# Performance work log

Hardware: AMD Instinct MI355X
Metric: run time of the kernel (lower is better)

The kernel has to match this reference:

```python
import jax, jax.numpy as jnp
import numpy as np

N_EXPERTS = 8
D_MODEL = 1024
D_FF = 2048
N_TOKENS = 4096
TOP_K = 2


def _init_expert_weight(key, shape):
    # matches torch init: bound = sqrt(3) * (sqrt(1/3)/sqrt(fan_in)) = 1/sqrt(fan_in)
    fan_in = shape[1]
    bound = 1.0 / np.sqrt(fan_in)
    return jax.random.uniform(key, shape, dtype=jnp.float32, minval=-bound, maxval=bound)


def setup_inputs() -> dict:
    key = jax.random.key(0)
    k_x, k_idx, k_w, k1, k2, k3 = jax.random.split(key, 6)
    x = jax.random.normal(k_x, (N_TOKENS, D_MODEL), dtype=jnp.float32)
    expert_indices = jax.random.randint(k_idx, (N_TOKENS, TOP_K), 0, N_EXPERTS)
    expert_weights = jax.random.uniform(k_w, (N_TOKENS, TOP_K), dtype=jnp.float32)
    w1 = _init_expert_weight(k1, (N_EXPERTS, D_MODEL, D_FF))
    w2 = _init_expert_weight(k2, (N_EXPERTS, D_MODEL, D_FF))
    w3 = _init_expert_weight(k3, (N_EXPERTS, D_FF, D_MODEL))
    return {"x": x, "expert_indices": expert_indices, "expert_weights": expert_weights,
            "w1": w1, "w2": w2, "w3": w3}


def reference(x, expert_indices, expert_weights, w1, w2, w3):
    # SwiGLU per expert, computed densely over all (token, expert) pairs,
    # then the top-k selected expert outputs are gathered and combined.
    # Mathematically identical to the padded-bmm dispatch/combine in the source.
    gate = jax.nn.silu(jnp.einsum('td,edf->tef', x, w1))   # [T, E, F]
    value = jnp.einsum('td,edf->tef', x, w2)               # [T, E, F]
    hidden = gate * value                                  # [T, E, F]
    out_e = jnp.einsum('tef,efd->ted', hidden, w3)         # [T, E, D]
    # gather each token's top-k expert outputs: [T, K, D]
    sel = jnp.take_along_axis(out_e, expert_indices[:, :, None], axis=1)
    return jnp.sum(sel * expert_weights[:, :, None], axis=1)  # [T, D]
```

## Files before the change

### kernel.cpp

```cpp
#include <hip/hip_runtime.h>
#include <hip/hip_bf16.h>

#define N_TOK   4096
#define DM      1024
#define DF      2048
#define NEXP    8
#define NPAIR   (N_TOK * 2)
#define BM      128
#define BN      128
#define BK      32
#define LDK     40

typedef __attribute__((ext_vector_type(8))) short bf16x8;
typedef __attribute__((ext_vector_type(4))) float f32x4;

__device__ __forceinline__ unsigned short to_bf16(float f) {
    unsigned u = __builtin_bit_cast(unsigned, f);
    unsigned r = (u + 0x7FFFu + ((u >> 16) & 1u)) >> 16;
    return (unsigned short)r;
}
__device__ __forceinline__ unsigned pk_bf16(float a, float b) {
    return (unsigned)to_bf16(a) | ((unsigned)to_bf16(b) << 16);
}
__device__ __forceinline__ void gld16(const unsigned short* g, unsigned short* l) {
    __builtin_amdgcn_global_load_lds(
        (const __attribute__((address_space(1))) unsigned int*)(g),
        (__attribute__((address_space(3))) unsigned int*)(l), 16, 0, 0);
}

__global__ void k_count(const int* __restrict__ eidx, int* __restrict__ meta) {
    int i = blockIdx.x * 256 + threadIdx.x;
    if (i < NPAIR) atomicAdd(&meta[eidx[i] & 7], 1);
}
__global__ void k_scan(int* __restrict__ meta) {
    if (threadIdx.x == 0) {
        int off = 0, mt = 0;
        for (int e = 0; e < NEXP; ++e) {
            meta[16 + e] = off; meta[25 + e] = mt;
            int c = meta[e];
            off += c; mt += (c + BM - 1) / BM;
        }
        meta[16 + NEXP] = off; meta[25 + NEXP] = mt; meta[34] = mt;
    }
}
__global__ void k_scatter(const int* __restrict__ eidx, int* __restrict__ meta,
                          int* __restrict__ rows) {
    int i = blockIdx.x * 256 + threadIdx.x;
    if (i < NPAIR) {
        int e = eidx[i] & 7;
        int p = meta[16 + e] + atomicAdd(&meta[8 + e], 1);
        rows[p] = i;
    }
}

__global__ __launch_bounds__(256)
void k_cvt_x(const float* __restrict__ x, unsigned short* __restrict__ xb) {
    int i = (blockIdx.x * 256 + threadIdx.x) * 8;
    float4 v0 = *(const float4*)(x + i);
    float4 v1 = *(const float4*)(x + i + 4);
    uint4 w;
    w.x = pk_bf16(v0.x, v0.y); w.y = pk_bf16(v0.z, v0.w);
    w.z = pk_bf16(v1.x, v1.y); w.w = pk_bf16(v1.z, v1.w);
    *(uint4*)(xb + i) = w;
}

__global__ __launch_bounds__(256)
void k_transpose(const float* __restrict__ src, unsigned short* __restrict__ dst,
                 int K, int F) {
    __shared__ __align__(16) unsigned short tile[64 * 80];
    const int e  = blockIdx.z;
    const int k0 = blockIdx.y * 64;
    const int f0 = blockIdx.x * 64;
    const int t  = threadIdx.x;
    const float* s = src + (size_t)e * K * F;
    unsigned short* d = dst + (size_t)e * K * F;
    const int fi = t & 63;
    const int kg = t >> 6;
    #pragma unroll
    for (int i = 0; i < 16; ++i) {
        int k = kg * 16 + i;
        tile[k * 80 + fi] = to_bf16(s[(size_t)(k0 + k) * F + f0 + fi]);
    }
    __syncthreads();
    const int kc = (t & 7) * 8;
    const int fo = t >> 3;
    #pragma unroll
    for (int j = 0; j < 2; ++j) {
        int f = fo + j * 32;
        unsigned short v[8];
        #pragma unroll
        for (int i = 0; i < 8; ++i) v[i] = tile[(kc + i) * 80 + f];
        uint4 w;
        w.x = (unsigned)v[0] | ((unsigned)v[1] << 16);
        w.y = (unsigned)v[2] | ((unsigned)v[3] << 16);
        w.z = (unsigned)v[4] | ((unsigned)v[5] << 16);
        w.w = (unsigned)v[6] | ((unsigned)v[7] << 16);
        *(uint4*)&d[(size_t)(f0 + f) * K + k0 + kc] = w;
    }
}

__global__ __launch_bounds__(256, 2)
void k_gemm1_bf(const unsigned short* __restrict__ xb,
                const unsigned short* __restrict__ w1t,
                const unsigned short* __restrict__ w2t,
                const int* __restrict__ meta,
                const int* __restrict__ rows,
                unsigned short* __restrict__ H)
{
    __shared__ __align__(16) unsigned short As [BM * BK];
    __shared__ __align__(16) unsigned short B1s[BN * BK];
    __shared__ __align__(16) unsigned short B2s[BN * BK];
    __shared__ int s_tok[BM];

    const int mt = blockIdx.y;
    if (mt >= meta[34]) return;
    int e = 0;
    #pragma unroll
    for (int i = 0; i < NEXP - 1; ++i) if (mt >= meta[25 + i + 1]) e = i + 1;
    const int rowEnd = meta[16 + e + 1];
    const int row0   = meta[16 + e] + (mt - meta[25 + e]) * BM;
    const int f0     = blockIdx.x * BN;
    const int tid    = threadIdx.x;

    if (tid < BM) {
        int gr = row0 + tid;
        s_tok[tid] = (gr < rowEnd) ? (rows[gr] >> 1) : 0;
    }
    __syncthreads();

    const int lane = tid & 63;
    const int wave = tid >> 6;
    const int r0 = wave * 32 + (lane >> 2);
    const int r1 = r0 + 16;
    const int kb = (lane & 3) * 8;
    const unsigned short* a_src0 = xb + (size_t)s_tok[r0] * DM + kb;
    const unsigned short* a_src1 = xb + (size_t)s_tok[r1] * DM + kb;
    const size_t wb = (size_t)e * DM * DF;
    const unsigned short* b1_src0 = w1t + wb + (size_t)(f0 + r0) * DM + kb;
    const unsigned short* b1_src1 = w1t + wb + (size_t)(f0 + r1) * DM + kb;
    const unsigned short* b2_src0 = w2t + wb + (size_t)(f0 + r0) * DM + kb;
    const unsigned short* b2_src1 = w2t + wb + (size_t)(f0 + r1) * DM + kb;
    unsigned short* As0  = &As [wave * 1024];
    unsigned short* As1  = &As [wave * 1024 + 512];
    unsigned short* B1s0 = &B1s[wave * 1024];
    unsigned short* B1s1 = &B1s[wave * 1024 + 512];
    unsigned short* B2s0 = &B2s[wave * 1024];
    unsigned short* B2s1 = &B2s[wave * 1024 + 512];

    f32x4 accg[4][4], accv[4][4];
    #pragma unroll
    for (int i = 0; i < 4; ++i)
        #pragma unroll
        for (int j = 0; j < 4; ++j) { accg[i][j] = (f32x4)0.f; accv[i][j] = (f32x4)0.f; }

    const int wm = (wave >> 1) * 64;
    const int wn = (wave & 1) * 64;
    const int am = lane & 15;
    const int ak = (lane >> 4) * 8;

    for (int k0 = 0; k0 < DM; k0 += BK) {
        gld16(a_src0 + k0, As0);
        gld16(a_src1 + k0, As1);
        gld16(b1_src0 + k0, B1s0);
        gld16(b1_src1 + k0, B1s1);
        gld16(b2_src0 + k0, B2s0);
        gld16(b2_src1 + k0, B2s1);
        __syncthreads();

        bf16x8 a[4], b1[4], b2[4];
        #pragma unroll
        for (int mi = 0; mi < 4; ++mi) a[mi] = *(const bf16x8*)&As[(wm + mi * 16 + am) * BK + ak];
        #pragma unroll
        for (int ni = 0; ni < 4; ++ni) {
            b1[ni] = *(const bf16x8*)&B1s[(wn + ni * 16 + am) * BK + ak];
            b2[ni] = *(const bf16x8*)&B2s[(wn + ni * 16 + am) * BK + ak];
        }
        #pragma unroll
        for (int mi = 0; mi < 4; ++mi)
            #pragma unroll
            for (int ni = 0; ni < 4; ++ni) {
                accg[mi][ni] = __builtin_amdgcn_mfma_f32_16x16x32_bf16(a[mi], b1[ni], accg[mi][ni], 0, 0, 0);
                accv[mi][ni] = __builtin_amdgcn_mfma_f32_16x16x32_bf16(a[mi], b2[ni], accv[mi][ni], 0, 0, 0);
            }
        __syncthreads();
    }

    const int cn = lane & 15;
    const int cq = (lane >> 4) * 4;
    #pragma unroll
    for (int mi = 0; mi < 4; ++mi) {
        #pragma unroll
        for (int r = 0; r < 4; ++r) {
            const int row = wm + mi * 16 + cq + r;
            const int gr  = row0 + row;
            if (gr < rowEnd) {
                unsigned short* dst = H + (size_t)gr * DF + f0 + wn;
                #pragma unroll
                for (int ni = 0; ni < 4; ++ni) {
                    float g = accg[mi][ni][r];
                    float v = accv[mi][ni][r];
                    float h = (g * v) / (1.f + __expf(-g));
                    dst[ni * 16 + cn] = to_bf16(h);
                }
            }
        }
    }
}

__global__ __launch_bounds__(256, 2)
void k_gemm2_bf(const unsigned short* __restrict__ H,
                const unsigned short* __restrict__ w3t,
                const int* __restrict__ meta,
                const int* __restrict__ rows,
                const float* __restrict__ ew,
                float* __restrict__ out)
{
    __shared__ __align__(16) unsigned short As[BM * BK];
    __shared__ __align__(16) unsigned short Bs[BN * BK];
    __shared__ int   s_tok[BM];
    __shared__ float s_w[BM];

    const int mt = blockIdx.y;
    if (mt >= meta[34]) return;
    int e = 0;
    #pragma unroll
    for (int i = 0; i < NEXP - 1; ++i) if (mt >= meta[25 + i + 1]) e = i + 1;
    const int rowEnd = meta[16 + e + 1];
    const int row0   = meta[16 + e] + (mt - meta[25 + e]) * BM;
    const int d0     = blockIdx.x * BN;
    const int tid    = threadIdx.x;

    if (tid < BM) {
        int gr = row0 + tid;
        if (gr < rowEnd) { int pr = rows[gr]; s_tok[tid] = pr >> 1; s_w[tid] = ew[pr]; }
        else             { s_tok[tid] = 0;    s_w[tid] = 0.f; }
    }
    __syncthreads();

    const int lane = tid & 63;
    const int wave = tid >> 6;
    const int r0 = wave * 32 + (lane >> 2);
    const int r1 = r0 + 16;
    const int kb = (lane & 3) * 8;
    int gr0 = row0 + r0; if (gr0 > NPAIR - 1) gr0 = NPAIR - 1;
    int gr1 = row0 + r1; if (gr1 > NPAIR - 1) gr1 = NPAIR - 1;
    const unsigned short* a_src0 = H + (size_t)gr0 * DF + kb;
    const unsigned short* a_src1 = H + (size_t)gr1 * DF + kb;
    const size_t wb = (size_t)e * DM * DF;
    const unsigned short* b_src0 = w3t + wb + (size_t)(d0 + r0) * DF + kb;
    const unsigned short* b_src1 = w3t + wb + (size_t)(d0 + r1) * DF + kb;
    unsigned short* As0 = &As[wave * 1024];
    unsigned short* As1 = &As[wave * 1024 + 512];
    unsigned short* Bs0 = &Bs[wave * 1024];
    unsigned short* Bs1 = &Bs[wave * 1024 + 512];

    f32x4 acc[4][4];
    #pragma unroll
    for (int i = 0; i < 4; ++i)
        #pragma unroll
        for (int j = 0; j < 4; ++j) acc[i][j] = (f32x4)0.f;

    const int wm = (wave >> 1) * 64;
    const int wn = (wave & 1) * 64;
    const int am = lane & 15;
    const int ak = (lane >> 4) * 8;

    for (int k0 = 0; k0 < DF; k0 += BK) {
        gld16(a_src0 + k0, As0);
        gld16(a_src1 + k0, As1);
        gld16(b_src0 + k0, Bs0);
        gld16(b_src1 + k0, Bs1);
        __syncthreads();

        bf16x8 a[4], b[4];
        #pragma unroll
        for (int mi = 0; mi < 4; ++mi) a[mi] = *(const bf16x8*)&As[(wm + mi * 16 + am) * BK + ak];
        #pragma unroll
        for (int ni = 0; ni < 4; ++ni) b[ni] = *(const bf16x8*)&Bs[(wn + ni * 16 + am) * BK + ak];
        #pragma unroll
        for (int mi = 0; mi < 4; ++mi)
            #pragma unroll
            for (int ni = 0; ni < 4; ++ni)
                acc[mi][ni] = __builtin_amdgcn_mfma_f32_16x16x32_bf16(a[mi], b[ni], acc[mi][ni], 0, 0, 0);
        __syncthreads();
    }

    const int cn = lane & 15;
    const int cq = (lane >> 4) * 4;
    #pragma unroll
    for (int mi = 0; mi < 4; ++mi) {
        #pragma unroll
        for (int r = 0; r < 4; ++r) {
            const int row = wm + mi * 16 + cq + r;
            const int gr  = row0 + row;
            if (gr < rowEnd) {
                const int   tok = s_tok[row];
                const float wgt = s_w[row];
                float* dst = out + (size_t)tok * DM + d0 + wn;
                #pragma unroll
                for (int ni = 0; ni < 4; ++ni)
                    atomicAdd(&dst[ni * 16 + cn], wgt * acc[mi][ni][r]);
            }
        }
    }
}

__global__ __launch_bounds__(256, 2)
void k_gemm1(const float* __restrict__ x, const float* __restrict__ w1,
             const float* __restrict__ w2, const int* __restrict__ meta,
             const int* __restrict__ rows, unsigned short* __restrict__ H)
{
    __shared__ unsigned short As[BM][LDK];
    __shared__ unsigned short B1s[BN][LDK];
    __shared__ unsigned short B2s[BN][LDK];
    __shared__ int s_tok[BM];
    const int mt = blockIdx.y;
    if (mt >= meta[34]) return;
    int e = 0;
    #pragma unroll
    for (int i = 0; i < NEXP - 1; ++i) if (mt >= meta[25 + i + 1]) e = i + 1;
    const int rowEnd = meta[16 + e + 1];
    const int row0   = meta[16 + e] + (mt - meta[25 + e]) * BM;
    const int f0     = blockIdx.x * BN;
    const int tid    = threadIdx.x;
    if (tid < BM) {
        int gr = row0 + tid;
        s_tok[tid] = (gr < rowEnd) ? (rows[gr] >> 1) : -1;
    }
    __syncthreads();
    const int ar = tid >> 1;
    const int ah = (tid & 1) * 16;
    const int a_tok = s_tok[ar];
    const float* a_src = x + (size_t)(a_tok < 0 ? 0 : a_tok) * DM + ah;
    const int bn_ = tid & 127;
    const int bk_ = (tid >> 7) * 16;
    const float* b1_src = w1 + (size_t)e * DM * DF + (size_t)bk_ * DF + f0 + bn_;
    const float* b2_src = w2 + (size_t)e * DM * DF + (size_t)bk_ * DF + f0 + bn_;
    f32x4 accg[4][4], accv[4][4];
    #pragma unroll
    for (int i = 0; i < 4; ++i)
        #pragma unroll
        for (int j = 0; j < 4; ++j) { accg[i][j] = (f32x4)0.f; accv[i][j] = (f32x4)0.f; }
    const int lane = tid & 63;
    const int wave = tid >> 6;
    const int wm = (wave >> 1) * 64;
    const int wn = (wave & 1) * 64;
    const int am = lane & 15;
    const int ak = (lane >> 4) * 8;
    for (int k0 = 0; k0 < DM; k0 += BK) {
        {
            const float* p = a_src + k0;
            #pragma unroll
            for (int jj = 0; jj < 4; ++jj) {
                float4 v;
                if (a_tok < 0) { v.x = v.y = v.z = v.w = 0.f; }
                else           { v = *(const float4*)(p + jj * 4); }
                uint2 w;
                w.x = pk_bf16(v.x, v.y); w.y = pk_bf16(v.z, v.w);
                *(uint2*)&As[ar][ah + jj * 4] = w;
            }
        }
        {
            const float* p1 = b1_src + (size_t)k0 * DF;
            const float* p2 = b2_src + (size_t)k0 * DF;
            #pragma unroll
            for (int c = 0; c < 2; ++c) {
                float v[8];
                #pragma unroll
                for (int j = 0; j < 8; ++j) v[j] = p1[(size_t)(c * 8 + j) * DF];
                uint4 w;
                w.x = pk_bf16(v[0], v[1]); w.y = pk_bf16(v[2], v[3]);
                w.z = pk_bf16(v[4], v[5]); w.w = pk_bf16(v[6], v[7]);
                *(uint4*)&B1s[bn_][bk_ + c * 8] = w;
            }
            #pragma unroll
            for (int c = 0; c < 2; ++c) {
                float v[8];
                #pragma unroll
                for (int j = 0; j < 8; ++j) v[j] = p2[(size_t)(c * 8 + j) * DF];
                uint4 w;
                w.x = pk_bf16(v[0], v[1]); w.y = pk_bf16(v[2], v[3]);
                w.z = pk_bf16(v[4], v[5]); w.w = pk_bf16(v[6], v[7]);
                *(uint4*)&B2s[bn_][bk_ + c * 8] = w;
            }
        }
        __syncthreads();
        bf16x8 a[4], b1[4], b2[4];
        #pragma unroll
        for (int mi = 0; mi < 4; ++mi) a[mi] = *(const bf16x8*)&As[wm + mi * 16 + am][ak];
        #pragma unroll
        for (int ni = 0; ni < 4; ++ni) {
            b1[ni] = *(const bf16x8*)&B1s[wn + ni * 16 + am][ak];
            b2[ni] = *(const bf16x8*)&B2s[wn + ni * 16 + am][ak];
        }
        #pragma unroll
        for (int mi = 0; mi < 4; ++mi)
            #pragma unroll
            for (int ni = 0; ni < 4; ++ni) {
                accg[mi][ni] = __builtin_amdgcn_mfma_f32_16x16x32_bf16(a[mi], b1[ni], accg[mi][ni], 0, 0, 0);
                accv[mi][ni] = __builtin_amdgcn_mfma_f32_16x16x32_bf16(a[mi], b2[ni], accv[mi][ni], 0, 0, 0);
            }
        __syncthreads();
    }
    const int cn = lane & 15;
    const int cq = (lane >> 4) * 4;
    #pragma unroll
    for (int mi = 0; mi < 4; ++mi) {
        #pragma unroll
        for (int r = 0; r < 4; ++r) {
            const int row = wm + mi * 16 + cq + r;
            const int gr  = row0 + row;
            if (gr < rowEnd) {
                unsigned short* dst = H + (size_t)gr * DF + f0 + wn;
                #pragma unroll
                for (int ni = 0; ni < 4; ++ni) {
                    float g = accg[mi][ni][r];
                    float v = accv[mi][ni][r];
                    float h = (g * v) / (1.f + __expf(-g));
                    dst[ni * 16 + cn] = to_bf16(h);
                }
            }
        }
    }
}

__global__ __launch_bounds__(256, 2)
void k_gemm2(const unsigned short* __restrict__ H, const float* __restrict__ w3,
             const int* __restrict__ meta, const int* __restrict__ rows,
             const float* __restrict__ ew, float* __restrict__ out)
{
    __shared__ unsigned short As[BM][LDK];
    __shared__ unsigned short Bs[BN][LDK];
    __shared__ int   s_tok[BM];
    __shared__ float s_w[BM];
    const int mt = blockIdx.y;
    if (mt >= meta[34]) return;
    int e = 0;
    #pragma unroll
    for (int i = 0; i < NEXP - 1; ++i) if (mt >= meta[25 + i + 1]) e = i + 1;
    const int rowEnd = meta[16 + e + 1];
    const int row0   = meta[16 + e] + (mt - meta[25 + e]) * BM;
    const int d0     = blockIdx.x * BN;
    const int tid    = threadIdx.x;
    if (tid < BM) {
        int gr = row0 + tid;
        if (gr < rowEnd) { int pr = rows[gr]; s_tok[tid] = pr >> 1; s_w[tid] = ew[pr]; }
        else             { s_tok[tid] = 0;    s_w[tid] = 0.f; }
    }
    __syncthreads();
    const int ar = tid >> 1;
    const int ah = (tid & 1) * 16;
    int a_row = row0 + ar; if (a_row >= NPAIR) a_row = NPAIR - 1;
    const unsigned short* a_src = H + (size_t)a_row * DF + ah;
    const int bn_ = tid & 127;
    const int bk_ = (tid >> 7) * 16;
    const float* b_src = w3 + (size_t)e * DF * DM + (size_t)bk_ * DM + d0 + bn_;
    f32x4 acc[4][4];
    #pragma unroll
    for (int i = 0; i < 4; ++i)
        #pragma unroll
        for (int j = 0; j < 4; ++j) acc[i][j] = (f32x4)0.f;
    const int lane = tid & 63;
    const int wave = tid >> 6;
    const int wm = (wave >> 1) * 64;
    const int wn = (wave & 1) * 64;
    const int am = lane & 15;
    const int ak = (lane >> 4) * 8;
    for (int k0 = 0; k0 < DF; k0 += BK) {
        *(uint4*)&As[ar][ah]     = *(const uint4*)(a_src + k0);
        *(uint4*)&As[ar][ah + 8] = *(const uint4*)(a_src + k0 + 8);
        {
            const float* p = b_src + (size_t)k0 * DM;
            #pragma unroll
            for (int c = 0; c < 2; ++c) {
                float v[8];
                #pragma unroll
                for (int j = 0; j < 8; ++j) v[j] = p[(size_t)(c * 8 + j) * DM];
                uint4 w;
                w.x = pk_bf16(v[0], v[1]); w.y = pk_bf16(v[2], v[3]);
                w.z = pk_bf16(v[4], v[5]); w.w = pk_bf16(v[6], v[7]);
                *(uint4*)&Bs[bn_][bk_ + c * 8] = w;
            }
        }
        __syncthreads();
        bf16x8 a[4], b[4];
        #pragma unroll
        for (int mi = 0; mi < 4; ++mi) a[mi] = *(const bf16x8*)&As[wm + mi * 16 + am][ak];
        #pragma unroll
        for (int ni = 0; ni < 4; ++ni) b[ni] = *(const bf16x8*)&Bs[wn + ni * 16 + am][ak];
        #pragma unroll
        for (int mi = 0; mi < 4; ++mi)
            #pragma unroll
            for (int ni = 0; ni < 4; ++ni)
                acc[mi][ni] = __builtin_amdgcn_mfma_f32_16x16x32_bf16(a[mi], b[ni], acc[mi][ni], 0, 0, 0);
        __syncthreads();
    }
    const int cn = lane & 15;
    const int cq = (lane >> 4) * 4;
    #pragma unroll
    for (int mi = 0; mi < 4; ++mi) {
        #pragma unroll
        for (int r = 0; r < 4; ++r) {
            const int row = wm + mi * 16 + cq + r;
            const int gr  = row0 + row;
            if (gr < rowEnd) {
                const int   tok = s_tok[row];
                const float wgt = s_w[row];
                float* dst = out + (size_t)tok * DM + d0 + wn;
                #pragma unroll
                for (int ni = 0; ni < 4; ++ni)
                    atomicAdd(&dst[ni * 16 + cn], wgt * acc[mi][ni][r]);
            }
        }
    }
}

__global__ __launch_bounds__(256)
void k_fallback(const float* __restrict__ x, const int* __restrict__ eidx,
                const float* __restrict__ ew, const float* __restrict__ w1,
                const float* __restrict__ w2, const float* __restrict__ w3,
                float* __restrict__ out)
{
    __shared__ float xs[DM];
    __shared__ float hs[DF];
    const int pair = blockIdx.x;
    const int t = pair >> 1;
    const int e = eidx[pair] & 7;
    const float wgt = ew[pair];
    const int tid = threadIdx.x;
    for (int i = tid; i < DM; i += 256) xs[i] = x[(size_t)t * DM + i];
    __syncthreads();
    for (int f = tid; f < DF; f += 256) {
        const float* c1 = w1 + (size_t)e * DM * DF + f;
        const float* c2 = w2 + (size_t)e * DM * DF + f;
        float g = 0.f, v = 0.f;
        for (int d = 0; d < DM; ++d) {
            float xv = xs[d];
            g += xv * c1[(size_t)d * DF];
            v += xv * c2[(size_t)d * DF];
        }
        hs[f] = (g * v) / (1.f + __expf(-g));
    }
    __syncthreads();
    for (int d = tid; d < DM; d += 256) {
        const float* c3 = w3 + (size_t)e * DF * DM + d;
        float o = 0.f;
        for (int f = 0; f < DF; ++f) o += hs[f] * c3[(size_t)f * DM];
        atomicAdd(&out[(size_t)t * DM + d], wgt * o);
    }
}

extern "C" void kernel_launch(void* const* d_in, const int* in_sizes, int n_in,
                              void* d_out, int out_size, void* d_ws, size_t ws_size,
                              hipStream_t stream)
{
    const float* x  = (const float*)d_in[0];
    const int*   ei = (const int*)  d_in[1];
    const float* ew = (const float*)d_in[2];
    const float* w1 = (const float*)d_in[3];
    const float* w2 = (const float*)d_in[4];
    const float* w3 = (const float*)d_in[5];
    float* out = (float*)d_out;

    (void)hipMemsetAsync(d_out, 0, (size_t)out_size * sizeof(float), stream);

    const size_t SZ_H  = (size_t)NPAIR * DF * 2;
    const size_t SZ_XB = (size_t)N_TOK * DM * 2;
    const size_t SZ_W  = (size_t)NEXP * DM * DF * 2;
    const size_t OFF_H  = 65536;
    const size_t OFF_XB = OFF_H + SZ_H;
    const size_t OFF_W1 = OFF_XB + SZ_XB;
    const size_t OFF_W2 = OFF_W1 + SZ_W;
    const size_t OFF_W3 = OFF_W2 + SZ_W;
    const size_t NEED_BIG   = OFF_W3 + SZ_W;
    const size_t NEED_SMALL = OFF_H + SZ_H;

    if (ws_size < NEED_SMALL) {
        k_fallback<<<NPAIR, 256, 0, stream>>>(x, ei, ew, w1, w2, w3, out);
        return;
    }

    int* meta = (int*)d_ws;
    int* rows = meta + 64;
    unsigned short* H = (unsigned short*)((char*)d_ws + OFF_H);

    (void)hipMemsetAsync(d_ws, 0, 64, stream);
    k_count  <<<NPAIR / 256, 256, 0, stream>>>(ei, meta);
    k_scan   <<<1, 64, 0, stream>>>(meta);
    k_scatter<<<NPAIR / 256, 256, 0, stream>>>(ei, meta, rows);

    if (ws_size >= NEED_BIG) {
        unsigned short* xb  = (unsigned short*)((char*)d_ws + OFF_XB);
        unsigned short* w1t = (unsigned short*)((char*)d_ws + OFF_W1);
        unsigned short* w2t = (unsigned short*)((char*)d_ws + OFF_W2);
        unsigned short* w3t = (unsigned short*)((char*)d_ws + OFF_W3);
        k_cvt_x<<<(N_TOK * DM) / 2048, 256, 0, stream>>>(x, xb);
        k_transpose<<<dim3(DF / 64, DM / 64, NEXP), 256, 0, stream>>>(w1, w1t, DM, DF);
        k_transpose<<<dim3(DF / 64, DM / 64, NEXP), 256, 0, stream>>>(w2, w2t, DM, DF);
        k_transpose<<<dim3(DM / 64, DF / 64, NEXP), 256, 0, stream>>>(w3, w3t, DF, DM);
        k_gemm1_bf<<<dim3(DF / BN, NPAIR / BM + NEXP), 256, 0, stream>>>(xb, w1t, w2t, meta, rows, H);
        k_gemm2_bf<<<dim3(DM / BN, NPAIR / BM + NEXP), 256, 0, stream>>>(H, w3t, meta, rows, ew, out);
    } else {
        k_gemm1<<<dim3(DF / BN, NPAIR / BM + NEXP), 256, 0, stream>>>(x, w1, w2, meta, rows, H);
        k_gemm2<<<dim3(DM / BN, NPAIR / BM + NEXP), 256, 0, stream>>>(H, w3, meta, rows, ew, out);
    }
}
```

Baseline: 490.3 us.

## Replace atomic combine with per-pair output buffer, fuse count/scan, vectorize transpose

```diff
diff --git a/kernel.cpp b/kernel.cpp
--- a/kernel.cpp
+++ b/kernel.cpp
@@ -28,28 +28,37 @@
         (__attribute__((address_space(3))) unsigned int*)(l), 16, 0, 0);
 }
 
-__global__ void k_count(const int* __restrict__ eidx, int* __restrict__ meta) {
-    int i = blockIdx.x * 256 + threadIdx.x;
-    if (i < NPAIR) atomicAdd(&meta[eidx[i] & 7], 1);
-}
-__global__ void k_scan(int* __restrict__ meta) {
-    if (threadIdx.x == 0) {
+__global__ __launch_bounds__(256)
+void k_countscan(const int* __restrict__ eidx, int* __restrict__ meta) {
+    __shared__ int hist[NEXP];
+    const int t = threadIdx.x;
+    if (t < NEXP) hist[t] = 0;
+    __syncthreads();
+    unsigned long long h = 0;
+    for (int i = t; i < NPAIR; i += 256) h += 1ull << ((eidx[i] & 7) * 8);
+    #pragma unroll
+    for (int e = 0; e < NEXP; ++e) {
+        int c = (int)((h >> (e * 8)) & 0xFF);
+        if (c) atomicAdd(&hist[e], c);
+    }
+    __syncthreads();
+    if (t == 0) {
         int off = 0, mt = 0;
         for (int e = 0; e < NEXP; ++e) {
-            meta[16 + e] = off; meta[25 + e] = mt;
-            int c = meta[e];
-            off += c; mt += (c + BM - 1) / BM;
+            meta[16 + e] = off; meta[25 + e] = mt; meta[8 + e] = 0;
+            off += hist[e]; mt += (hist[e] + BM - 1) / BM;
         }
         meta[16 + NEXP] = off; meta[25 + NEXP] = mt; meta[34] = mt;
     }
 }
 __global__ void k_scatter(const int* __restrict__ eidx, int* __restrict__ meta,
-                          int* __restrict__ rows) {
+                          int* __restrict__ rows, int* __restrict__ inv) {
     int i = blockIdx.x * 256 + threadIdx.x;
     if (i < NPAIR) {
         int e = eidx[i] & 7;
         int p = meta[16 + e] + atomicAdd(&meta[8 + e], 1);
         rows[p] = i;
+        inv[i] = p;
     }
 }
 
@@ -74,12 +83,16 @@
     const int t  = threadIdx.x;
     const float* s = src + (size_t)e * K * F;
     unsigned short* d = dst + (size_t)e * K * F;
-    const int fi = t & 63;
-    const int kg = t >> 6;
-    #pragma unroll
-    for (int i = 0; i < 16; ++i) {
-        int k = kg * 16 + i;
-        tile[k * 80 + fi] = to_bf16(s[(size_t)(k0 + k) * F + f0 + fi]);
+    const int fq = (t & 15) * 4;
+    const int kr = t >> 4;
+    #pragma unroll
+    for (int j = 0; j < 4; ++j) {
+        int k = kr + j * 16;
+        float4 v = *(const float4*)&s[(size_t)(k0 + k) * F + f0 + fq];
+        uint2 w;
+        w.x = pk_bf16(v.x, v.y);
+        w.y = pk_bf16(v.z, v.w);
+        *(uint2*)&tile[k * 80 + fq] = w;
     }
     __syncthreads();
     const int kc = (t & 7) * 8;
@@ -99,7 +112,7 @@
     }
 }
 
-__global__ __launch_bounds__(256, 2)
+__global__ __launch_bounds__(256, 3)
 void k_gemm1_bf(const unsigned short* __restrict__ xb,
                 const unsigned short* __restrict__ w1t,
                 const unsigned short* __restrict__ w2t,
@@ -207,17 +220,16 @@
     }
 }
 
-__global__ __launch_bounds__(256, 2)
+__global__ __launch_bounds__(256, 3)
 void k_gemm2_bf(const unsigned short* __restrict__ H,
                 const unsigned short* __restrict__ w3t,
                 const int* __restrict__ meta,
                 const int* __restrict__ rows,
                 const float* __restrict__ ew,
-                float* __restrict__ out)
+                float* __restrict__ O)
 {
     __shared__ __align__(16) unsigned short As[BM * BK];
     __shared__ __align__(16) unsigned short Bs[BN * BK];
-    __shared__ int   s_tok[BM];
     __shared__ float s_w[BM];
 
     const int mt = blockIdx.y;
@@ -232,8 +244,7 @@
 
     if (tid < BM) {
         int gr = row0 + tid;
-        if (gr < rowEnd) { int pr = rows[gr]; s_tok[tid] = pr >> 1; s_w[tid] = ew[pr]; }
-        else             { s_tok[tid] = 0;    s_w[tid] = 0.f; }
+        s_w[tid] = (gr < rowEnd) ? ew[rows[gr]] : 0.f;
     }
     __syncthreads();
 
@@ -294,15 +305,28 @@
             const int row = wm + mi * 16 + cq + r;
             const int gr  = row0 + row;
             if (gr < rowEnd) {
-                const int   tok = s_tok[row];
                 const float wgt = s_w[row];
-                float* dst = out + (size_t)tok * DM + d0 + wn;
+                float* dst = O + (size_t)gr * DM + d0 + wn;
                 #pragma unroll
                 for (int ni = 0; ni < 4; ++ni)
-                    atomicAdd(&dst[ni * 16 + cn], wgt * acc[mi][ni][r]);
-            }
-        }
-    }
+                    dst[ni * 16 + cn] = wgt * acc[mi][ni][r];
+            }
+        }
+    }
+}
+
+__global__ __launch_bounds__(256)
+void k_combine(const float* __restrict__ O, const int* __restrict__ inv,
+               float* __restrict__ out) {
+    const int t = blockIdx.x;
+    const int d = threadIdx.x * 4;
+    const int p0 = inv[2 * t];
+    const int p1 = inv[2 * t + 1];
+    float4 a = *(const float4*)(O + (size_t)p0 * DM + d);
+    float4 b = *(const float4*)(O + (size_t)p1 * DM + d);
+    float4 r;
+    r.x = a.x + b.x; r.y = a.y + b.y; r.z = a.z + b.z; r.w = a.w + b.w;
+    *(float4*)(out + (size_t)t * DM + d) = r;
 }
 
 __global__ __launch_bounds__(256, 2)
@@ -562,12 +586,10 @@
     const float* w3 = (const float*)d_in[5];
     float* out = (float*)d_out;
 
-    (void)hipMemsetAsync(d_out, 0, (size_t)out_size * sizeof(float), stream);
-
     const size_t SZ_H  = (size_t)NPAIR * DF * 2;
     const size_t SZ_XB = (size_t)N_TOK * DM * 2;
     const size_t SZ_W  = (size_t)NEXP * DM * DF * 2;
-    const size_t OFF_H  = 65536;
+    const size_t OFF_H  = 131072;
     const size_t OFF_XB = OFF_H + SZ_H;
     const size_t OFF_W1 = OFF_XB + SZ_XB;
     const size_t OFF_W2 = OFF_W1 + SZ_W;
@@ -576,31 +598,34 @@
     const size_t NEED_SMALL = OFF_H + SZ_H;
 
     if (ws_size < NEED_SMALL) {
+        (void)hipMemsetAsync(d_out, 0, (size_t)out_size * sizeof(float), stream);
         k_fallback<<<NPAIR, 256, 0, stream>>>(x, ei, ew, w1, w2, w3, out);
         return;
     }
 
     int* meta = (int*)d_ws;
-    int* rows = meta + 64;
+    int* rows = (int*)((char*)d_ws + 256);
+    int* inv  = (int*)((char*)d_ws + 256 + 32768);
     unsigned short* H = (unsigned short*)((char*)d_ws + OFF_H);
 
-    (void)hipMemsetAsync(d_ws, 0, 64, stream);
-    k_count  <<<NPAIR / 256, 256, 0, stream>>>(ei, meta);
-    k_scan   <<<1, 64, 0, stream>>>(meta);
-    k_scatter<<<NPAIR / 256, 256, 0, stream>>>(ei, meta, rows);
+    k_countscan<<<1, 256, 0, stream>>>(ei, meta);
+    k_scatter  <<<NPAIR / 256, 256, 0, stream>>>(ei, meta, rows, inv);
 
     if (ws_size >= NEED_BIG) {
         unsigned short* xb  = (unsigned short*)((char*)d_ws + OFF_XB);
         unsigned short* w1t = (unsigned short*)((char*)d_ws + OFF_W1);
         unsigned short* w2t = (unsigned short*)((char*)d_ws + OFF_W2);
         unsigned short* w3t = (unsigned short*)((char*)d_ws + OFF_W3);
+        float*          O   = (float*)((char*)d_ws + OFF_W1);
         k_cvt_x<<<(N_TOK * DM) / 2048, 256, 0, stream>>>(x, xb);
         k_transpose<<<dim3(DF / 64, DM / 64, NEXP), 256, 0, stream>>>(w1, w1t, DM, DF);
         k_transpose<<<dim3(DF / 64, DM / 64, NEXP), 256, 0, stream>>>(w2, w2t, DM, DF);
         k_transpose<<<dim3(DM / 64, DF / 64, NEXP), 256, 0, stream>>>(w3, w3t, DF, DM);
         k_gemm1_bf<<<dim3(DF / BN, NPAIR / BM + NEXP), 256, 0, stream>>>(xb, w1t, w2t, meta, rows, H);
-        k_gemm2_bf<<<dim3(DM / BN, NPAIR / BM + NEXP), 256, 0, stream>>>(H, w3t, meta, rows, ew, out);
+        k_gemm2_bf<<<dim3(DM / BN, NPAIR / BM + NEXP), 256, 0, stream>>>(H, w3t, meta, rows, ew, O);
+        k_combine <<<N_TOK, 256, 0, stream>>>(O, inv, out);
     } else {
+        (void)hipMemsetAsync(d_out, 0, (size_t)out_size * sizeof(float), stream);
         k_gemm1<<<dim3(DF / BN, NPAIR / BM + NEXP), 256, 0, stream>>>(x, w1, w2, meta, rows, H);
         k_gemm2<<<dim3(DM / BN, NPAIR / BM + NEXP), 256, 0, stream>>>(H, w3, meta, rows, ew, out);
     }
```

Result: slower. 844.6 us (+72.3%).
